# Performance work log

Hardware: AMD Instinct MI355X
Metric: run time of the kernel (lower is better)

The kernel has to match this reference:

```python
import jax, jax.numpy as jnp
import numpy as np

N_QUBITS = 12
DEPTH = 2
TOPOLOGY = 'ring'
N_FEATURES = 12
BATCH = 4096
DIM = 2 ** N_QUBITS


def _apply_ry(state, theta):
    # state: [B, left, 2, right] caller-reshaped; here take [B, 2**n] + qubit index
    return state


def apply_ry(state, theta, q):
    # RY(theta) = [[cos(t/2), -sin(t/2)], [sin(t/2), cos(t/2)]], shared across batch
    c, s = jnp.cos(theta / 2), jnp.sin(theta / 2)
    G = jnp.stack([jnp.stack([c, -s]), jnp.stack([s, c])])  # [2, 2]
    left = 2 ** q
    right = 2 ** (N_QUBITS - q - 1)
    st = state.reshape(-1, left, 2, right)
    st = jnp.einsum('ab,xlbr->xlar', G, st)
    return st.reshape(state.shape)


def apply_cnot(state, c, t):
    # flip target axis on the control=1 half of the statevector
    B = state.shape[0]
    st = state.reshape((B,) + (2,) * N_QUBITS)
    c_ax, t_ax = 1 + c, 1 + t
    s0 = jnp.take(st, 0, axis=c_ax)
    s1 = jnp.take(st, 1, axis=c_ax)
    t_adj = t_ax if t < c else t_ax - 1  # axis shift after removing control axis
    s1 = jnp.flip(s1, axis=t_adj)
    st = jnp.stack([s0, s1], axis=c_ax)
    return st.reshape(B, DIM)


def circuit_features(x, weights):
    B = x.shape[0]
    # initial layer: RY(x[i % n_features]) on |0> per qubit -> product state
    idx = np.arange(N_QUBITS) % N_FEATURES
    half = x[:, idx] / 2  # [B, n_qubits]
    state = jnp.ones((B, 1), dtype=x.dtype)
    for i in range(N_QUBITS):
        v = jnp.stack([jnp.cos(half[:, i]), jnp.sin(half[:, i])], axis=1)  # [B, 2]
        state = (state[:, :, None] * v[:, None, :]).reshape(B, -1)
    # entangling + trainable RY layers
    for l in range(DEPTH):
        if TOPOLOGY == 'ring':
            pairs = [(i, (i + 1) % N_QUBITS) for i in range(N_QUBITS)]
        elif TOPOLOGY == 'chain':
            pairs = [(i, i + 1) for i in range(N_QUBITS - 1)]
        else:  # all2all
            pairs = [(i, j) for i in range(N_QUBITS) for j in range(i + 1, N_QUBITS)]
        for (ci, ti) in pairs:
            state = apply_cnot(state, ci, ti)
        for i in range(N_QUBITS):
            state = apply_ry(state, weights[l, i], i)
    # <Z_i> = sum_b |amp_b|^2 * (1 - 2*bit_i(b)); qubit 0 is most significant
    probs = state * state  # [B, 2^n], state is real
    bits = (np.arange(DIM)[None, :] >> (N_QUBITS - 1 - np.arange(N_QUBITS))[:, None]) & 1
    signs = jnp.asarray(1.0 - 2.0 * bits, dtype=x.dtype)  # [n_qubits, 2^n]
    return probs @ signs.T  # [B, n_qubits]


def setup_inputs() -> dict:
    key = jax.random.key(0)
    kx, kw, kW, kb = jax.random.split(key, 4)
    x = jax.random.normal(kx, (BATCH, N_FEATURES), dtype=jnp.float32)
    weights = jax.random.normal(kw, (DEPTH, N_QUBITS), dtype=jnp.float32)
    W = jax.random.normal(kW, (2, N_QUBITS), dtype=jnp.float32) / np.sqrt(N_QUBITS)
    b = jnp.zeros((2,), dtype=jnp.float32)
    return {"x": x, "weights": weights, "W": W, "b": b}


def reference(x, weights, W, b):
    feats = circuit_features(x, weights)  # [B, n_qubits]
    return feats @ W.T + b  # [B, 2]
```

## Files before the change

kernel.cpp:

```cpp
#include <hip/hip_runtime.h>
#include <hip/hip_bf16.h>

#define NQ 12
typedef __hip_bfloat16 bf16;

__device__ __forceinline__ float b2f(unsigned int u) {
  union { unsigned int i; float f; } v; v.i = u << 16; return v.f;
}

__device__ __forceinline__ float ldv(const void* p, int i, bool f32) {
  if (f32) return ((const float*)p)[i];
  return b2f((unsigned int)((const unsigned short*)p)[i]);
}

__device__ __forceinline__ int ringperm(int d) {
  int a = d ^ ((d & 1) << 11);
  return a ^ (a >> 1);
}

__device__ __forceinline__ int swz(int p) { return p ^ ((p >> 6) & 31); }

__global__ __launch_bounds__(64) void qsim_kernel(
    const void* __restrict__ x,
    const void* __restrict__ w,
    const void* __restrict__ Wm,
    const void* __restrict__ bv,
    void* __restrict__ out)
{
  __shared__ float st[4096];
  const int lane = threadIdx.x;
  const int b = blockIdx.x;

  bool f32;
  {
    const unsigned short* xu = (const unsigned short*)x;
    int insane = 0;
#pragma unroll
    for (int i = 0; i < 16; ++i) {
      float v = b2f((unsigned int)xu[2 * i]);
      float a = fabsf(v);
      if (!(a <= 64.f) || (a != 0.f && a < 1e-8f)) ++insane;
    }
    f32 = (insane >= 2);
  }

  float lp = 1.f;
#pragma unroll
  for (int q = 6; q < 12; ++q) {
    float h = 0.5f * ldv(x, b * NQ + q, f32);
    lp *= ((lane >> (11 - q)) & 1) ? __sinf(h) : __cosf(h);
  }
  float amp[64];
  {
    float h0 = 0.5f * ldv(x, b * NQ + 0, f32);
    amp[0] = lp * __cosf(h0);
    amp[1] = lp * __sinf(h0);
#pragma unroll
    for (int lvl = 1; lvl < 6; ++lvl) {
      float h = 0.5f * ldv(x, b * NQ + lvl, f32);
      float cc = __cosf(h), ss = __sinf(h);
#pragma unroll
      for (int i = (1 << lvl) - 1; i >= 0; --i) {
        float t = amp[i];
        amp[2 * i]     = t * cc;
        amp[2 * i + 1] = t * ss;
      }
    }
  }

#pragma unroll 1
  for (int l = 0; l < 2; ++l) {
    __syncthreads();
#pragma unroll
    for (int j = 0; j < 64; ++j) st[((j << 6) ^ (j & 31)) ^ lane] = amp[j];
    __syncthreads();
    {
      const int rb = swz(ringperm(lane << 6));
#pragma unroll
      for (int j = 0; j < 64; ++j) amp[j] = st[rb ^ swz(ringperm(j))];
    }

#pragma unroll
    for (int q = 6; q < 12; ++q) {
      float h = 0.5f * ldv(w, l * NQ + q, f32);
      const float c = __cosf(h), s = __sinf(h);
      const int m = 1 << (11 - q);
#pragma unroll
      for (int j = 0; j < 64; ++j) {
        if (j & m) continue;
        float v0 = amp[j], v1 = amp[j | m];
        amp[j]     = fmaf(c, v0, -s * v1);
        amp[j | m] = fmaf(s, v0,  c * v1);
      }
    }

    __syncthreads();
    {
      const int wb = (lane << 6) ^ (lane & 31);
#pragma unroll
      for (int j = 0; j < 64; ++j) st[wb ^ j] = amp[j];
    }
    __syncthreads();
#pragma unroll
    for (int j = 0; j < 64; ++j) amp[j] = st[((j << 6) ^ (j & 31)) ^ lane];

#pragma unroll
    for (int q = 0; q < 6; ++q) {
      float h = 0.5f * ldv(w, l * NQ + q, f32);
      const float c = __cosf(h), s = __sinf(h);
      const int m = 1 << (5 - q);
#pragma unroll
      for (int j = 0; j < 64; ++j) {
        if (j & m) continue;
        float v0 = amp[j], v1 = amp[j | m];
        amp[j]     = fmaf(c, v0, -s * v1);
        amp[j | m] = fmaf(s, v0,  c * v1);
      }
    }
  }

  float P = 0.f, z0 = 0.f, z1 = 0.f, z2 = 0.f, z3 = 0.f, z4 = 0.f, z5 = 0.f;
#pragma unroll
  for (int j = 0; j < 64; ++j) {
    float pr = amp[j] * amp[j];
    P  += pr;
    z0 += (j & 32) ? -pr : pr;
    z1 += (j & 16) ? -pr : pr;
    z2 += (j & 8)  ? -pr : pr;
    z3 += (j & 4)  ? -pr : pr;
    z4 += (j & 2)  ? -pr : pr;
    z5 += (j & 1)  ? -pr : pr;
  }

  float t0, t1;
#pragma unroll
  for (int r = 0; r < 2; ++r) {
    float acc = z0 * ldv(Wm, r * NQ + 0, f32) + z1 * ldv(Wm, r * NQ + 1, f32)
              + z2 * ldv(Wm, r * NQ + 2, f32) + z3 * ldv(Wm, r * NQ + 3, f32)
              + z4 * ldv(Wm, r * NQ + 4, f32) + z5 * ldv(Wm, r * NQ + 5, f32);
    float wsum = 0.f;
#pragma unroll
    for (int q = 6; q < 12; ++q) {
      float wv = ldv(Wm, r * NQ + q, f32);
      wsum += ((lane >> (11 - q)) & 1) ? -wv : wv;
    }
    acc = fmaf(P, wsum, acc);
    if (r == 0) t0 = acc; else t1 = acc;
  }
#pragma unroll
  for (int off = 32; off; off >>= 1) {
    t0 += __shfl_xor(t0, off, 64);
    t1 += __shfl_xor(t1, off, 64);
  }
  if (lane < 2) {
    float o = ((lane == 0) ? t0 : t1) + ldv(bv, lane, f32);
    if (f32) ((float*)out)[b * 2 + lane] = o;
    else     ((bf16*)out)[b * 2 + lane] = __float2bfloat16(o);
  }
}

extern "C" void kernel_launch(void* const* d_in, const int* in_sizes, int n_in,
                              void* d_out, int out_size, void* d_ws, size_t ws_size,
                              hipStream_t stream) {
  const void* x  = d_in[0];
  const void* w  = d_in[1];
  const void* Wm = d_in[2];
  const void* bv = d_in[3];
  const int batch = out_size / 2;
  qsim_kernel<<<dim3(batch), dim3(64), 0, stream>>>(x, w, Wm, bv, d_out);
}
```

Baseline: 95.89 us.

## Split statevector across two waves with 32 amplitudes per thread

Each block now uses 128 threads (two waves), and each thread holds 32 amplitudes instead of 64. Gates on qubits 5 and 6 in the transposed phase are applied with cross-lane shuffles rather than in registers. The shared-memory swizzle is adapted to the new layout, and the final reduction combines the two waves through shared memory. This lowers register pressure and doubles the threads per state to raise occupancy and parallelism, at the cost of shuffle traffic and an extra barrier.

```diff
diff --git a/kernel.cpp b/kernel.cpp
--- a/kernel.cpp
+++ b/kernel.cpp
@@ -18,9 +18,9 @@
   return a ^ (a >> 1);
 }
 
-__device__ __forceinline__ int swz(int p) { return p ^ ((p >> 6) & 31); }
+__device__ __forceinline__ int swz5(int p) { return p ^ ((p >> 5) & 31); }
 
-__global__ __launch_bounds__(64) void qsim_kernel(
+__global__ __launch_bounds__(128) void qsim_kernel(
     const void* __restrict__ x,
     const void* __restrict__ w,
     const void* __restrict__ Wm,
@@ -28,7 +28,9 @@
     void* __restrict__ out)
 {
   __shared__ float st[4096];
-  const int lane = threadIdx.x;
+  const int t = threadIdx.x;
+  const int lane = t & 63;
+  const int wave = t >> 6;
   const int b = blockIdx.x;
 
   bool f32;
@@ -46,71 +48,78 @@
 
   float lp = 1.f;
 #pragma unroll
-  for (int q = 6; q < 12; ++q) {
+  for (int q = 5; q < 12; ++q) {
     float h = 0.5f * ldv(x, b * NQ + q, f32);
-    lp *= ((lane >> (11 - q)) & 1) ? __sinf(h) : __cosf(h);
+    lp *= ((t >> (11 - q)) & 1) ? __sinf(h) : __cosf(h);
   }
-  float amp[64];
-  {
-    float h0 = 0.5f * ldv(x, b * NQ + 0, f32);
-    amp[0] = lp * __cosf(h0);
-    amp[1] = lp * __sinf(h0);
+  float amp[32];
+  amp[0] = lp;
 #pragma unroll
-    for (int lvl = 1; lvl < 6; ++lvl) {
-      float h = 0.5f * ldv(x, b * NQ + lvl, f32);
-      float cc = __cosf(h), ss = __sinf(h);
+  for (int q = 0; q < 5; ++q) {
+    float h = 0.5f * ldv(x, b * NQ + q, f32);
+    float c = __cosf(h), s = __sinf(h);
+    const int m = 1 << (4 - q);
 #pragma unroll
-      for (int i = (1 << lvl) - 1; i >= 0; --i) {
-        float t = amp[i];
-        amp[2 * i]     = t * cc;
-        amp[2 * i + 1] = t * ss;
-      }
+    for (int j = 0; j < 32; j += 2 * m) {
+      float a0 = amp[j];
+      amp[j]     = a0 * c;
+      amp[j | m] = a0 * s;
     }
   }
+
+  const int wA = swz5(t);
+  const int rB = swz5(ringperm(t << 5));
+  const int wB = swz5(t << 5);
 
 #pragma unroll 1
   for (int l = 0; l < 2; ++l) {
     __syncthreads();
 #pragma unroll
-    for (int j = 0; j < 64; ++j) st[((j << 6) ^ (j & 31)) ^ lane] = amp[j];
+    for (int j = 0; j < 32; ++j) st[swz5(j << 7) ^ wA] = amp[j];
     __syncthreads();
-    {
-      const int rb = swz(ringperm(lane << 6));
 #pragma unroll
-      for (int j = 0; j < 64; ++j) amp[j] = st[rb ^ swz(ringperm(j))];
-    }
+    for (int j = 0; j < 32; ++j) amp[j] = st[rB ^ swz5(ringperm(j))];
 
 #pragma unroll
-    for (int q = 6; q < 12; ++q) {
+    for (int q = 7; q < 12; ++q) {
       float h = 0.5f * ldv(w, l * NQ + q, f32);
       const float c = __cosf(h), s = __sinf(h);
       const int m = 1 << (11 - q);
 #pragma unroll
-      for (int j = 0; j < 64; ++j) {
+      for (int j = 0; j < 32; ++j) {
         if (j & m) continue;
         float v0 = amp[j], v1 = amp[j | m];
         amp[j]     = fmaf(c, v0, -s * v1);
         amp[j | m] = fmaf(s, v0,  c * v1);
       }
     }
+#pragma unroll
+    for (int q = 5; q < 7; ++q) {
+      float h = 0.5f * ldv(w, l * NQ + q, f32);
+      const float c = __cosf(h), s = __sinf(h);
+      const int lm = (q == 5) ? 2 : 1;
+      const float se = (lane & lm) ? s : -s;
+#pragma unroll
+      for (int j = 0; j < 32; ++j) {
+        float o = __shfl_xor(amp[j], lm, 64);
+        amp[j] = fmaf(c, amp[j], se * o);
+      }
+    }
 
     __syncthreads();
-    {
-      const int wb = (lane << 6) ^ (lane & 31);
 #pragma unroll
-      for (int j = 0; j < 64; ++j) st[wb ^ j] = amp[j];
-    }
+    for (int j = 0; j < 32; ++j) st[wB ^ j] = amp[j];
     __syncthreads();
 #pragma unroll
-    for (int j = 0; j < 64; ++j) amp[j] = st[((j << 6) ^ (j & 31)) ^ lane];
+    for (int j = 0; j < 32; ++j) amp[j] = st[swz5(j << 7) ^ wA];
 
 #pragma unroll
-    for (int q = 0; q < 6; ++q) {
+    for (int q = 0; q < 5; ++q) {
       float h = 0.5f * ldv(w, l * NQ + q, f32);
       const float c = __cosf(h), s = __sinf(h);
-      const int m = 1 << (5 - q);
+      const int m = 1 << (4 - q);
 #pragma unroll
-      for (int j = 0; j < 64; ++j) {
+      for (int j = 0; j < 32; ++j) {
         if (j & m) continue;
         float v0 = amp[j], v1 = amp[j | m];
         amp[j]     = fmaf(c, v0, -s * v1);
@@ -119,43 +128,45 @@
     }
   }
 
-  float P = 0.f, z0 = 0.f, z1 = 0.f, z2 = 0.f, z3 = 0.f, z4 = 0.f, z5 = 0.f;
+  float P = 0.f, z0 = 0.f, z1 = 0.f, z2 = 0.f, z3 = 0.f, z4 = 0.f;
 #pragma unroll
-  for (int j = 0; j < 64; ++j) {
+  for (int j = 0; j < 32; ++j) {
     float pr = amp[j] * amp[j];
     P  += pr;
-    z0 += (j & 32) ? -pr : pr;
-    z1 += (j & 16) ? -pr : pr;
-    z2 += (j & 8)  ? -pr : pr;
-    z3 += (j & 4)  ? -pr : pr;
-    z4 += (j & 2)  ? -pr : pr;
-    z5 += (j & 1)  ? -pr : pr;
+    z0 += (j & 16) ? -pr : pr;
+    z1 += (j & 8)  ? -pr : pr;
+    z2 += (j & 4)  ? -pr : pr;
+    z3 += (j & 2)  ? -pr : pr;
+    z4 += (j & 1)  ? -pr : pr;
   }
 
-  float t0, t1;
+  float acc0, acc1;
 #pragma unroll
   for (int r = 0; r < 2; ++r) {
-    float acc = z0 * ldv(Wm, r * NQ + 0, f32) + z1 * ldv(Wm, r * NQ + 1, f32)
-              + z2 * ldv(Wm, r * NQ + 2, f32) + z3 * ldv(Wm, r * NQ + 3, f32)
-              + z4 * ldv(Wm, r * NQ + 4, f32) + z5 * ldv(Wm, r * NQ + 5, f32);
-    float wsum = 0.f;
+    float a = z0 * ldv(Wm, r * NQ + 0, f32) + z1 * ldv(Wm, r * NQ + 1, f32)
+            + z2 * ldv(Wm, r * NQ + 2, f32) + z3 * ldv(Wm, r * NQ + 3, f32)
+            + z4 * ldv(Wm, r * NQ + 4, f32);
+    float ws = 0.f;
 #pragma unroll
-    for (int q = 6; q < 12; ++q) {
+    for (int q = 5; q < 12; ++q) {
       float wv = ldv(Wm, r * NQ + q, f32);
-      wsum += ((lane >> (11 - q)) & 1) ? -wv : wv;
+      ws += ((t >> (11 - q)) & 1) ? -wv : wv;
     }
-    acc = fmaf(P, wsum, acc);
-    if (r == 0) t0 = acc; else t1 = acc;
+    float v = fmaf(P, ws, a);
+    if (r == 0) acc0 = v; else acc1 = v;
   }
 #pragma unroll
   for (int off = 32; off; off >>= 1) {
-    t0 += __shfl_xor(t0, off, 64);
-    t1 += __shfl_xor(t1, off, 64);
+    acc0 += __shfl_xor(acc0, off, 64);
+    acc1 += __shfl_xor(acc1, off, 64);
   }
-  if (lane < 2) {
-    float o = ((lane == 0) ? t0 : t1) + ldv(bv, lane, f32);
-    if (f32) ((float*)out)[b * 2 + lane] = o;
-    else     ((bf16*)out)[b * 2 + lane] = __float2bfloat16(o);
+  __syncthreads();
+  if (lane == 0) { st[wave * 2 + 0] = acc0; st[wave * 2 + 1] = acc1; }
+  __syncthreads();
+  if (t < 2) {
+    float o = st[t] + st[2 + t] + ldv(bv, t, f32);
+    if (f32) ((float*)out)[b * 2 + t] = o;
+    else     ((bf16*)out)[b * 2 + t] = __float2bfloat16(o);
   }
 }
 
@@ -167,5 +178,5 @@
   const void* Wm = d_in[2];
   const void* bv = d_in[3];
   const int batch = out_size / 2;
-  qsim_kernel<<<dim3(batch), dim3(64), 0, stream>>>(x, w, Wm, bv, d_out);
+  qsim_kernel<<<dim3(batch), dim3(128), 0, stream>>>(x, w, Wm, bv, d_out);
 }
```

Measured after the change: 103.0 us. 1.07x slower.

## Process two batch samples per 64-thread block to amortize setup and syncs

Applied to the files above, without the earlier changes.

Each block now simulates two batch elements, holding both 64-amplitude register arrays and reusing the precomputed gate cos/sin values and the shared-memory transpose buffer serially. This halves the grid size and amortizes per-block overheads such as the dtype detection, weight trig and launch cost. In exchange it doubles register usage to at least 128 amplitude registers per thread, which lowers occupancy or risks spills, and adds extra barriers for the serialized transposes. It also assumes an even batch size.

```diff
diff --git a/kernel.cpp b/kernel.cpp
--- a/kernel.cpp
+++ b/kernel.cpp
@@ -19,6 +19,30 @@
 }
 
 __device__ __forceinline__ int swz(int p) { return p ^ ((p >> 6) & 31); }
+
+__device__ __forceinline__ void init_state(const void* x, int bb, bool f32,
+                                           int lane, float (&amp)[64]) {
+  float lp = 1.f;
+#pragma unroll
+  for (int q = 6; q < 12; ++q) {
+    float h = 0.5f * ldv(x, bb * NQ + q, f32);
+    lp *= ((lane >> (11 - q)) & 1) ? __sinf(h) : __cosf(h);
+  }
+  float h0 = 0.5f * ldv(x, bb * NQ + 0, f32);
+  amp[0] = lp * __cosf(h0);
+  amp[1] = lp * __sinf(h0);
+#pragma unroll
+  for (int lvl = 1; lvl < 6; ++lvl) {
+    float h = 0.5f * ldv(x, bb * NQ + lvl, f32);
+    float cc = __cosf(h), ss = __sinf(h);
+#pragma unroll
+    for (int i = (1 << lvl) - 1; i >= 0; --i) {
+      float t = amp[i];
+      amp[2 * i]     = t * cc;
+      amp[2 * i + 1] = t * ss;
+    }
+  }
+}
 
 __global__ __launch_bounds__(64) void qsim_kernel(
     const void* __restrict__ x,
@@ -29,7 +53,8 @@
 {
   __shared__ float st[4096];
   const int lane = threadIdx.x;
-  const int b = blockIdx.x;
+  const int bA = 2 * blockIdx.x;
+  const int bB = bA + 1;
 
   bool f32;
   {
@@ -44,118 +69,153 @@
     f32 = (insane >= 2);
   }
 
-  float lp = 1.f;
-#pragma unroll
-  for (int q = 6; q < 12; ++q) {
-    float h = 0.5f * ldv(x, b * NQ + q, f32);
-    lp *= ((lane >> (11 - q)) & 1) ? __sinf(h) : __cosf(h);
-  }
-  float amp[64];
-  {
-    float h0 = 0.5f * ldv(x, b * NQ + 0, f32);
-    amp[0] = lp * __cosf(h0);
-    amp[1] = lp * __sinf(h0);
-#pragma unroll
-    for (int lvl = 1; lvl < 6; ++lvl) {
-      float h = 0.5f * ldv(x, b * NQ + lvl, f32);
-      float cc = __cosf(h), ss = __sinf(h);
-#pragma unroll
-      for (int i = (1 << lvl) - 1; i >= 0; --i) {
-        float t = amp[i];
-        amp[2 * i]     = t * cc;
-        amp[2 * i + 1] = t * ss;
-      }
-    }
-  }
+  float ampA[64], ampB[64];
+  init_state(x, bA, f32, lane, ampA);
+  init_state(x, bB, f32, lane, ampB);
+
+  const int rb1 = swz(ringperm(lane << 6));
+  const int wb2 = (lane << 6) ^ (lane & 31);
 
 #pragma unroll 1
   for (int l = 0; l < 2; ++l) {
     __syncthreads();
 #pragma unroll
-    for (int j = 0; j < 64; ++j) st[((j << 6) ^ (j & 31)) ^ lane] = amp[j];
-    __syncthreads();
-    {
-      const int rb = swz(ringperm(lane << 6));
-#pragma unroll
-      for (int j = 0; j < 64; ++j) amp[j] = st[rb ^ swz(ringperm(j))];
-    }
-
+    for (int j = 0; j < 64; ++j) st[((j << 6) ^ (j & 31)) ^ lane] = ampA[j];
+    __syncthreads();
+#pragma unroll
+    for (int j = 0; j < 64; ++j) ampA[j] = st[rb1 ^ swz(ringperm(j))];
+    __syncthreads();
+#pragma unroll
+    for (int j = 0; j < 64; ++j) st[((j << 6) ^ (j & 31)) ^ lane] = ampB[j];
+    __syncthreads();
+#pragma unroll
+    for (int j = 0; j < 64; ++j) ampB[j] = st[rb1 ^ swz(ringperm(j))];
+
+    float cch[6], ssh[6];
 #pragma unroll
     for (int q = 6; q < 12; ++q) {
       float h = 0.5f * ldv(w, l * NQ + q, f32);
-      const float c = __cosf(h), s = __sinf(h);
+      cch[q - 6] = __cosf(h); ssh[q - 6] = __sinf(h);
+    }
+#pragma unroll
+    for (int q = 6; q < 12; ++q) {
+      const float c = cch[q - 6], s = ssh[q - 6];
       const int m = 1 << (11 - q);
 #pragma unroll
       for (int j = 0; j < 64; ++j) {
         if (j & m) continue;
-        float v0 = amp[j], v1 = amp[j | m];
-        amp[j]     = fmaf(c, v0, -s * v1);
-        amp[j | m] = fmaf(s, v0,  c * v1);
-      }
-    }
-
-    __syncthreads();
-    {
-      const int wb = (lane << 6) ^ (lane & 31);
-#pragma unroll
-      for (int j = 0; j < 64; ++j) st[wb ^ j] = amp[j];
-    }
-    __syncthreads();
-#pragma unroll
-    for (int j = 0; j < 64; ++j) amp[j] = st[((j << 6) ^ (j & 31)) ^ lane];
+        float v0 = ampA[j], v1 = ampA[j | m];
+        ampA[j]     = fmaf(c, v0, -s * v1);
+        ampA[j | m] = fmaf(s, v0,  c * v1);
+      }
+    }
+#pragma unroll
+    for (int q = 6; q < 12; ++q) {
+      const float c = cch[q - 6], s = ssh[q - 6];
+      const int m = 1 << (11 - q);
+#pragma unroll
+      for (int j = 0; j < 64; ++j) {
+        if (j & m) continue;
+        float v0 = ampB[j], v1 = ampB[j | m];
+        ampB[j]     = fmaf(c, v0, -s * v1);
+        ampB[j | m] = fmaf(s, v0,  c * v1);
+      }
+    }
+
+    __syncthreads();
+#pragma unroll
+    for (int j = 0; j < 64; ++j) st[wb2 ^ j] = ampA[j];
+    __syncthreads();
+#pragma unroll
+    for (int j = 0; j < 64; ++j) ampA[j] = st[((j << 6) ^ (j & 31)) ^ lane];
+    __syncthreads();
+#pragma unroll
+    for (int j = 0; j < 64; ++j) st[wb2 ^ j] = ampB[j];
+    __syncthreads();
+#pragma unroll
+    for (int j = 0; j < 64; ++j) ampB[j] = st[((j << 6) ^ (j & 31)) ^ lane];
 
 #pragma unroll
     for (int q = 0; q < 6; ++q) {
       float h = 0.5f * ldv(w, l * NQ + q, f32);
-      const float c = __cosf(h), s = __sinf(h);
+      cch[q] = __cosf(h); ssh[q] = __sinf(h);
+    }
+#pragma unroll
+    for (int q = 0; q < 6; ++q) {
+      const float c = cch[q], s = ssh[q];
       const int m = 1 << (5 - q);
 #pragma unroll
       for (int j = 0; j < 64; ++j) {
         if (j & m) continue;
-        float v0 = amp[j], v1 = amp[j | m];
-        amp[j]     = fmaf(c, v0, -s * v1);
-        amp[j | m] = fmaf(s, v0,  c * v1);
-      }
-    }
-  }
-
-  float P = 0.f, z0 = 0.f, z1 = 0.f, z2 = 0.f, z3 = 0.f, z4 = 0.f, z5 = 0.f;
+        float v0 = ampA[j], v1 = ampA[j | m];
+        ampA[j]     = fmaf(c, v0, -s * v1);
+        ampA[j | m] = fmaf(s, v0,  c * v1);
+      }
+    }
+#pragma unroll
+    for (int q = 0; q < 6; ++q) {
+      const float c = cch[q], s = ssh[q];
+      const int m = 1 << (5 - q);
+#pragma unroll
+      for (int j = 0; j < 64; ++j) {
+        if (j & m) continue;
+        float v0 = ampB[j], v1 = ampB[j | m];
+        ampB[j]     = fmaf(c, v0, -s * v1);
+        ampB[j | m] = fmaf(s, v0,  c * v1);
+      }
+    }
+  }
+
+  float PA = 0.f, zA0 = 0.f, zA1 = 0.f, zA2 = 0.f, zA3 = 0.f, zA4 = 0.f, zA5 = 0.f;
+  float PB = 0.f, zB0 = 0.f, zB1 = 0.f, zB2 = 0.f, zB3 = 0.f, zB4 = 0.f, zB5 = 0.f;
 #pragma unroll
   for (int j = 0; j < 64; ++j) {
-    float pr = amp[j] * amp[j];
-    P  += pr;
-    z0 += (j & 32) ? -pr : pr;
-    z1 += (j & 16) ? -pr : pr;
-    z2 += (j & 8)  ? -pr : pr;
-    z3 += (j & 4)  ? -pr : pr;
-    z4 += (j & 2)  ? -pr : pr;
-    z5 += (j & 1)  ? -pr : pr;
-  }
-
-  float t0, t1;
+    float pa = ampA[j] * ampA[j];
+    float pb = ampB[j] * ampB[j];
+    PA += pa;                      PB += pb;
+    zA0 += (j & 32) ? -pa : pa;    zB0 += (j & 32) ? -pb : pb;
+    zA1 += (j & 16) ? -pa : pa;    zB1 += (j & 16) ? -pb : pb;
+    zA2 += (j & 8)  ? -pa : pa;    zB2 += (j & 8)  ? -pb : pb;
+    zA3 += (j & 4)  ? -pa : pa;    zB3 += (j & 4)  ? -pb : pb;
+    zA4 += (j & 2)  ? -pa : pa;    zB4 += (j & 2)  ? -pb : pb;
+    zA5 += (j & 1)  ? -pa : pa;    zB5 += (j & 1)  ? -pb : pb;
+  }
+
+  float tA0, tA1, tB0, tB1;
 #pragma unroll
   for (int r = 0; r < 2; ++r) {
-    float acc = z0 * ldv(Wm, r * NQ + 0, f32) + z1 * ldv(Wm, r * NQ + 1, f32)
-              + z2 * ldv(Wm, r * NQ + 2, f32) + z3 * ldv(Wm, r * NQ + 3, f32)
-              + z4 * ldv(Wm, r * NQ + 4, f32) + z5 * ldv(Wm, r * NQ + 5, f32);
+    float w0 = ldv(Wm, r * NQ + 0, f32), w1 = ldv(Wm, r * NQ + 1, f32),
+          w2 = ldv(Wm, r * NQ + 2, f32), w3 = ldv(Wm, r * NQ + 3, f32),
+          w4 = ldv(Wm, r * NQ + 4, f32), w5 = ldv(Wm, r * NQ + 5, f32);
+    float accA = zA0 * w0 + zA1 * w1 + zA2 * w2 + zA3 * w3 + zA4 * w4 + zA5 * w5;
+    float accB = zB0 * w0 + zB1 * w1 + zB2 * w2 + zB3 * w3 + zB4 * w4 + zB5 * w5;
     float wsum = 0.f;
 #pragma unroll
     for (int q = 6; q < 12; ++q) {
       float wv = ldv(Wm, r * NQ + q, f32);
       wsum += ((lane >> (11 - q)) & 1) ? -wv : wv;
     }
-    acc = fmaf(P, wsum, acc);
-    if (r == 0) t0 = acc; else t1 = acc;
+    accA = fmaf(PA, wsum, accA);
+    accB = fmaf(PB, wsum, accB);
+    if (r == 0) { tA0 = accA; tB0 = accB; }
+    else        { tA1 = accA; tB1 = accB; }
   }
 #pragma unroll
   for (int off = 32; off; off >>= 1) {
-    t0 += __shfl_xor(t0, off, 64);
-    t1 += __shfl_xor(t1, off, 64);
+    tA0 += __shfl_xor(tA0, off, 64);
+    tA1 += __shfl_xor(tA1, off, 64);
+    tB0 += __shfl_xor(tB0, off, 64);
+    tB1 += __shfl_xor(tB1, off, 64);
   }
   if (lane < 2) {
-    float o = ((lane == 0) ? t0 : t1) + ldv(bv, lane, f32);
-    if (f32) ((float*)out)[b * 2 + lane] = o;
-    else     ((bf16*)out)[b * 2 + lane] = __float2bfloat16(o);
+    float o = ((lane == 0) ? tA0 : tA1) + ldv(bv, lane, f32);
+    if (f32) ((float*)out)[bA * 2 + lane] = o;
+    else     ((bf16*)out)[bA * 2 + lane] = __float2bfloat16(o);
+  } else if (lane < 4) {
+    int r = lane - 2;
+    float o = ((r == 0) ? tB0 : tB1) + ldv(bv, r, f32);
+    if (f32) ((float*)out)[bB * 2 + r] = o;
+    else     ((bf16*)out)[bB * 2 + r] = __float2bfloat16(o);
   }
 }
 
@@ -167,5 +227,5 @@
   const void* Wm = d_in[2];
   const void* bv = d_in[3];
   const int batch = out_size / 2;
-  qsim_kernel<<<dim3(batch), dim3(64), 0, stream>>>(x, w, Wm, bv, d_out);
-}
+  qsim_kernel<<<dim3(batch / 2), dim3(64), 0, stream>>>(x, w, Wm, bv, d_out);
+}
```

After: 106.4 us. 1.11x slower.

## Build initial product state directly in ring-permuted layout, skip first LDS shuffle

Applied to the files above, without the earlier changes.

The initial product state is now computed per lane directly in the basis order that results after the first ring of CNOTs. Because the CNOT ring is a fixed permutation, each amplitude is a product of per-qubit cos/sin factors chosen by the permuted bits. This removes the first layer's shared-memory scatter/gather and its two barriers. In exchange it adds register pressure from the 12-entry factor arrays and a somewhat heavier initial product computation.

```diff
diff --git a/kernel.cpp b/kernel.cpp
--- a/kernel.cpp
+++ b/kernel.cpp
@@ -44,40 +44,67 @@
     f32 = (insane >= 2);
   }
 
-  float lp = 1.f;
-#pragma unroll
-  for (int q = 6; q < 12; ++q) {
-    float h = 0.5f * ldv(x, b * NQ + q, f32);
-    lp *= ((lane >> (11 - q)) & 1) ? __sinf(h) : __cosf(h);
-  }
   float amp[64];
   {
-    float h0 = 0.5f * ldv(x, b * NQ + 0, f32);
-    amp[0] = lp * __cosf(h0);
-    amp[1] = lp * __sinf(h0);
+    float csx[12], snx[12];
 #pragma unroll
-    for (int lvl = 1; lvl < 6; ++lvl) {
-      float h = 0.5f * ldv(x, b * NQ + lvl, f32);
-      float cc = __cosf(h), ss = __sinf(h);
+    for (int q = 0; q < 12; ++q) {
+      float h = 0.5f * ldv(x, b * NQ + q, f32);
+      csx[q] = __cosf(h); snx[q] = __sinf(h);
+    }
+    const int rb = ringperm(lane << 6);
+    float f0[12], f1[12];
 #pragma unroll
-      for (int i = (1 << lvl) - 1; i >= 0; --i) {
-        float t = amp[i];
-        amp[2 * i]     = t * cc;
-        amp[2 * i + 1] = t * ss;
+    for (int q = 0; q < 12; ++q) {
+      int r = (rb >> (11 - q)) & 1;
+      f0[q] = r ? snx[q] : csx[q];
+      f1[q] = r ? csx[q] : snx[q];
+    }
+    const float K   = f0[2] * f0[3] * f0[4] * f0[5];
+    const float h0f = f0[0] * f0[1];
+    const float h1f = f1[0] * f1[1];
+    const float u00 = f0[11] * h0f, u01 = f1[11] * h1f;
+    const float u10 = f1[11] * h0f, u11 = f0[11] * h1f;
+#pragma unroll
+    for (int j5 = 0; j5 < 2; ++j5) {
+      const float a5 = K * (j5 ? f1[6] : f0[6]);
+#pragma unroll
+      for (int j4 = 0; j4 < 2; ++j4) {
+        const float a4 = a5 * ((j4 ^ j5) ? f1[7] : f0[7]);
+#pragma unroll
+        for (int j3 = 0; j3 < 2; ++j3) {
+          const float a3 = a4 * ((j3 ^ j4) ? f1[8] : f0[8]);
+#pragma unroll
+          for (int j2 = 0; j2 < 2; ++j2) {
+            const float a2 = a3 * ((j2 ^ j3) ? f1[9] : f0[9]);
+#pragma unroll
+            for (int j1 = 0; j1 < 2; ++j1) {
+              const float a1 = a2 * ((j1 ^ j2) ? f1[10] : f0[10]);
+#pragma unroll
+              for (int j0 = 0; j0 < 2; ++j0) {
+                const float uu = j1 ? (j0 ? u11 : u10) : (j0 ? u01 : u00);
+                amp[(j5 << 5) | (j4 << 4) | (j3 << 3) | (j2 << 2) | (j1 << 1) | j0]
+                    = a1 * uu;
+              }
+            }
+          }
+        }
       }
     }
   }
 
+  const int rb1 = swz(ringperm(lane << 6));
+  const int wb2 = (lane << 6) ^ (lane & 31);
+
 #pragma unroll 1
   for (int l = 0; l < 2; ++l) {
-    __syncthreads();
+    if (l) {
+      __syncthreads();
 #pragma unroll
-    for (int j = 0; j < 64; ++j) st[((j << 6) ^ (j & 31)) ^ lane] = amp[j];
-    __syncthreads();
-    {
-      const int rb = swz(ringperm(lane << 6));
+      for (int j = 0; j < 64; ++j) st[((j << 6) ^ (j & 31)) ^ lane] = amp[j];
+      __syncthreads();
 #pragma unroll
-      for (int j = 0; j < 64; ++j) amp[j] = st[rb ^ swz(ringperm(j))];
+      for (int j = 0; j < 64; ++j) amp[j] = st[rb1 ^ swz(ringperm(j))];
     }
 
 #pragma unroll
@@ -95,11 +122,8 @@
     }
 
     __syncthreads();
-    {
-      const int wb = (lane << 6) ^ (lane & 31);
 #pragma unroll
-      for (int j = 0; j < 64; ++j) st[wb ^ j] = amp[j];
-    }
+    for (int j = 0; j < 64; ++j) st[wb2 ^ j] = amp[j];
     __syncthreads();
 #pragma unroll
     for (int j = 0; j < 64; ++j) amp[j] = st[((j << 6) ^ (j & 31)) ^ lane];
```

After: 95.09 us. Within noise of the previous version (-0.8%).
